# Performance work log

Measured on AMD Instinct MI355X. Metric: run time of the kernel, lower is better.

The kernel has to match this reference:

```python
import jax, jax.numpy as jnp
import numpy as np

B, T, D, H, Dh, ROT = 2, 2048, 2048, 16, 128, 64
DFF = 4 * D
EPS = 1e-5
NEG = -1e9


def setup_inputs() -> dict:
    key = jax.random.key(0)
    ks = jax.random.split(key, 8)
    s = lambda k, shape, sc: jax.random.normal(k, shape, jnp.float32) * sc
    return {
        "x": s(ks[0], (B, T, D), 1.0),
        "ln_scale": jnp.ones((D,), jnp.float32),
        "ln_offset": jnp.zeros((D,), jnp.float32),
        "wq": s(ks[1], (D, D), 0.02),
        "wk": s(ks[2], (D, D), 0.02),
        "wv": s(ks[3], (D, D), 0.02),
        "wo": s(ks[4], (D, D), 0.02),
        "w1": s(ks[5], (D, DFF), 0.02),
        "b1": jnp.zeros((DFF,), jnp.float32),
        "w2": s(ks[6], (DFF, D), 0.02),
        "b2": jnp.zeros((D,), jnp.float32),
    }


def reference(x, ln_scale, ln_offset, wq, wk, wv, wo, w1, b1, w2, b2):
    def ln(h):  # ReplicatedLayerNorm, fp32 internal; note: same params used twice (shared self.norm)
        h32 = h.astype(jnp.float32)
        m = jnp.mean(h32, axis=-1, keepdims=True)
        v = jnp.var(h32, axis=-1, keepdims=True)
        y = (h32 - m) * jax.lax.rsqrt(v + EPS)
        return (y * ln_scale + ln_offset).astype(h.dtype)

    xn = ln(x)
    q = (xn @ wq).reshape(B, T, H, Dh)
    k = (xn @ wk).reshape(B, T, H, Dh)
    v = (xn @ wv).reshape(B, T, H, Dh)

    # GPT-J interleaved RoPE on first ROT dims
    pos = jnp.arange(T, dtype=jnp.float32)
    inv_freq = 1.0 / (10000.0 ** (jnp.arange(0, ROT, 2, dtype=jnp.float32) / ROT))
    freqs = pos[:, None] * inv_freq[None, :]            # (T, ROT/2)
    cos = jnp.repeat(jnp.cos(freqs), 2, axis=-1)[None, :, None, :]  # (1,T,1,ROT)
    sin = jnp.repeat(jnp.sin(freqs), 2, axis=-1)[None, :, None, :]

    def rope(t):
        tr, tp = t[..., :ROT], t[..., ROT:]
        x1 = tr[..., 0::2]
        x2 = tr[..., 1::2]
        rot_half = jnp.stack((-x2, x1), axis=-1).reshape(tr.shape)
        return jnp.concatenate([tr * cos + rot_half * sin, tp], axis=-1)

    q, k = rope(q), rope(k)

    scale = 1.0 / jnp.sqrt(jnp.float32(Dh))
    scores = jnp.einsum('bthd,bshd->bhts', q, k) * scale
    mask = jnp.where(jnp.tril(jnp.ones((T, T), bool)), 0.0, NEG).astype(scores.dtype)
    w = jax.nn.softmax(scores + mask, axis=-1)
    ctx = jnp.einsum('bhts,bshd->bthd', w, v).reshape(B, T, D)
    x1_ = x + ctx @ wo

    xn2 = ln(x1_)
    h = jax.nn.gelu(xn2.astype(jnp.float32) @ w1 + b1)  # default approximate gelu, as in source
    ff = (h @ w2 + b2).astype(x.dtype)
    return x1_ + ff
```

## Files before the change

kernel.cpp:

```cpp
#include <hip/hip_runtime.h>
#include <hip/hip_bf16.h>

#define B_   2
#define T_   2048
#define D_   2048
#define H_   16
#define DH_  128
#define DFF_ 8192

typedef __attribute__((ext_vector_type(8))) short bf16x8;
typedef __attribute__((ext_vector_type(4))) float f32x4;

__device__ __forceinline__ short f2bf(float f) {
    __hip_bfloat16 h = __float2bfloat16(f);
    return *reinterpret_cast<short*>(&h);
}

__device__ __forceinline__ void gload_lds16(const void* g, void* l) {
    __builtin_amdgcn_global_load_lds(
        (const __attribute__((address_space(1))) void*)g,
        (__attribute__((address_space(3))) void*)l,
        16, 0, 0);
}

__device__ __forceinline__ float gelu_tanh(float x) {
    float x3 = x * x * x;
    return 0.5f * x * (1.f + tanhf(0.7978845608028654f * (x + 0.044715f * x3)));
}

#define MFMA32(a, b, c) __builtin_amdgcn_mfma_f32_16x16x32_bf16((a), (b), (c), 0, 0, 0)

__global__ __launch_bounds__(256) void transpose_cvt(const float* __restrict__ in,
                                                     __hip_bfloat16* __restrict__ out,
                                                     int K, int N, int out_ld, int out_row0)
{
    __shared__ float t[32][65];
    const int n0 = blockIdx.x * 64, k0 = blockIdx.y * 32;
    const int tid = threadIdx.x;
    {
        int kr = tid >> 4;
        int nc = (tid & 15) * 4;
        const float* src = in + (size_t)(k0 + kr) * N + n0 + nc;
        float4 a = *reinterpret_cast<const float4*>(src);
        float4 b = *reinterpret_cast<const float4*>(src + (size_t)16 * N);
        t[kr][nc] = a.x; t[kr][nc + 1] = a.y; t[kr][nc + 2] = a.z; t[kr][nc + 3] = a.w;
        t[kr + 16][nc] = b.x; t[kr + 16][nc + 1] = b.y; t[kr + 16][nc + 2] = b.z; t[kr + 16][nc + 3] = b.w;
    }
    __syncthreads();
    {
        int n  = tid >> 2;
        int kc = (tid & 3) * 8;
        __hip_bfloat16 ob[8];
#pragma unroll
        for (int j = 0; j < 8; ++j) ob[j] = __float2bfloat16(t[kc + j][n]);
        *reinterpret_cast<uint4*>(out + (size_t)(out_row0 + n0 + n) * out_ld + k0 + kc) =
            *reinterpret_cast<uint4*>(ob);
    }
}

__global__ __launch_bounds__(256) void ln_kernel(const float* __restrict__ x,
                                                 const float* __restrict__ sc,
                                                 const float* __restrict__ of,
                                                 __hip_bfloat16* __restrict__ out)
{
    int row = blockIdx.x, tid = threadIdx.x;
    const float* xr = x + (size_t)row * D_;
    float4 v0 = reinterpret_cast<const float4*>(xr)[tid * 2];
    float4 v1 = reinterpret_cast<const float4*>(xr)[tid * 2 + 1];
    float vv[8] = {v0.x, v0.y, v0.z, v0.w, v1.x, v1.y, v1.z, v1.w};
    float s = 0.f, ss = 0.f;
#pragma unroll
    for (int j = 0; j < 8; ++j) { s += vv[j]; ss += vv[j] * vv[j]; }
    for (int o = 32; o; o >>= 1) { s += __shfl_down(s, o); ss += __shfl_down(ss, o); }
    __shared__ float red[8];
    int wid = tid >> 6, lane = tid & 63;
    if (!lane) { red[wid] = s; red[4 + wid] = ss; }
    __syncthreads();
    s  = red[0] + red[1] + red[2] + red[3];
    ss = red[4] + red[5] + red[6] + red[7];
    float mean = s * (1.f / D_);
    float var  = ss * (1.f / D_) - mean * mean;
    float rstd = rsqrtf(var + 1e-5f);
    int c0 = tid * 8;
    __hip_bfloat16 ob[8];
#pragma unroll
    for (int j = 0; j < 8; ++j)
        ob[j] = __float2bfloat16((vv[j] - mean) * rstd * sc[c0 + j] + of[c0 + j]);
    *reinterpret_cast<uint4*>(out + (size_t)row * D_ + c0) = *reinterpret_cast<uint4*>(ob);
}

template<int EPI, int BM>
__global__ __launch_bounds__(512, 2) void gemm8p(
    const __hip_bfloat16* __restrict__ A, const __hip_bfloat16* __restrict__ BT,
    void* __restrict__ Cout, const float* __restrict__ bias,
    const float* __restrict__ resid, int M, int N, int K)
{
    constexpr int MFR = BM / 32;
    constexpr int AUL = BM / 128;
    constexpr int VMC = AUL + 2;
    __shared__ short As[2 * 2 * BM * 32];
    __shared__ short Bs[2 * 2 * 256 * 32];

    const int tid = threadIdx.x;
    const int wid = tid >> 6, lane = tid & 63;
    const int lo = lane & 15, hi = lane >> 4;
    const int wr = wid >> 2, wc = wid & 3;

    const int gx = gridDim.x;
    const int nwg = gx * gridDim.y;
    const int bid = blockIdx.y * gx + blockIdx.x;
    const int swz = (bid & 7) * (nwg >> 3) + (bid >> 3);
    const int m0 = (swz / gx) * BM, n0 = (swz % gx) * 256;

    auto stageA = [&](int tt, int ks) {
#pragma unroll
        for (int l = 0; l < AUL; ++l) {
            int c    = l * 512 + tid;
            int row  = c >> 2, ksub = c & 3;
            int kc   = tt * 64 + ks * 32 + ((ksub ^ ((row >> 1) & 3)) << 3);
            int c0   = l * 512 + wid * 64;
            gload_lds16(A + (size_t)(m0 + row) * K + kc,
                        (char*)As + ((tt & 1) * 2 + ks) * (BM * 64) + c0 * 16);
        }
    };
    auto stageB = [&](int tt, int ks) {
#pragma unroll
        for (int l = 0; l < 2; ++l) {
            int c    = l * 512 + tid;
            int row  = c >> 2, ksub = c & 3;
            int kc   = tt * 64 + ks * 32 + ((ksub ^ ((row >> 1) & 3)) << 3);
            int c0   = l * 512 + wid * 64;
            gload_lds16(BT + (size_t)(n0 + row) * K + kc,
                        (char*)Bs + ((tt & 1) * 2 + ks) * 16384 + c0 * 16);
        }
    };

    const int fsw  = (hi ^ ((lo >> 1) & 3)) << 4;
    const int arow = wr * (BM / 2) + lo;
    const int brow = wc * 64 + lo;

    f32x4 acc[MFR][4] = {};
    const int NT = K >> 6;

    stageA(0, 0); stageB(0, 0); stageA(0, 1); stageB(0, 1);
    asm volatile("s_waitcnt vmcnt(%0)" :: "i"(VMC) : "memory");
    __builtin_amdgcn_s_barrier();
    __builtin_amdgcn_sched_barrier(0);

#define PHASE_MFMA(J)                                                         \
        __builtin_amdgcn_s_barrier();                                         \
        asm volatile("s_waitcnt lgkmcnt(0)" ::: "memory");                    \
        __builtin_amdgcn_sched_barrier(0);                                    \
        __builtin_amdgcn_s_setprio(1);                                        \
        _Pragma("unroll")                                                     \
        for (int m = 0; m < MFR; ++m) {                                       \
            acc[m][J]     = MFMA32(af[m], b0, acc[m][J]);                     \
            acc[m][J + 1] = MFMA32(af[m], b1, acc[m][J + 1]);                 \
        }                                                                     \
        __builtin_amdgcn_s_setprio(0);

#pragma unroll 2
    for (int t = 0; t < NT; ++t) {
        const int bsel = t & 1;
        const bool pf = (t + 1 < NT);
        const char* Ab = (const char*)As + bsel * (2 * BM * 64);
        const char* Bb = (const char*)Bs + bsel * 32768;
        bf16x8 af[MFR], b0, b1;

#pragma unroll
        for (int m = 0; m < MFR; ++m)
            af[m] = *reinterpret_cast<const bf16x8*>(Ab + (arow + m * 16) * 64 + fsw);
        b0 = *reinterpret_cast<const bf16x8*>(Bb + brow * 64 + fsw);
        b1 = *reinterpret_cast<const bf16x8*>(Bb + (brow + 16) * 64 + fsw);
        if (pf) stageA(t + 1, 0);
        PHASE_MFMA(0)
        __builtin_amdgcn_s_barrier();
        __builtin_amdgcn_sched_barrier(0);

        b0 = *reinterpret_cast<const bf16x8*>(Bb + (brow + 32) * 64 + fsw);
        b1 = *reinterpret_cast<const bf16x8*>(Bb + (brow + 48) * 64 + fsw);
        if (pf) stageB(t + 1, 0);
        PHASE_MFMA(2)
        asm volatile("s_waitcnt vmcnt(%0)" :: "i"(VMC) : "memory");
        __builtin_amdgcn_s_barrier();
        __builtin_amdgcn_sched_barrier(0);

#pragma unroll
        for (int m = 0; m < MFR; ++m)
            af[m] = *reinterpret_cast<const bf16x8*>(Ab + BM * 64 + (arow + m * 16) * 64 + fsw);
        b0 = *reinterpret_cast<const bf16x8*>(Bb + 16384 + brow * 64 + fsw);
        b1 = *reinterpret_cast<const bf16x8*>(Bb + 16384 + (brow + 16) * 64 + fsw);
        if (pf) stageA(t + 1, 1);
        PHASE_MFMA(0)
        __builtin_amdgcn_s_barrier();
        __builtin_amdgcn_sched_barrier(0);

        b0 = *reinterpret_cast<const bf16x8*>(Bb + 16384 + (brow + 32) * 64 + fsw);
        b1 = *reinterpret_cast<const bf16x8*>(Bb + 16384 + (brow + 48) * 64 + fsw);
        if (pf) stageB(t + 1, 1);
        PHASE_MFMA(2)
        asm volatile("s_waitcnt vmcnt(%0)" :: "i"(VMC) : "memory");
        __builtin_amdgcn_s_barrier();
        __builtin_amdgcn_sched_barrier(0);
    }
#undef PHASE_MFMA

    float* Cf = (float*)Cout;
    __hip_bfloat16* Cb = (__hip_bfloat16*)Cout;
#pragma unroll
    for (int m = 0; m < MFR; ++m) {
        int rbase = m0 + wr * (BM / 2) + m * 16 + hi * 4;
#pragma unroll
        for (int j = 0; j < 4; ++j) {
            int col = n0 + wc * 64 + (j >> 1) * 32 + (j & 1) * 16 + lo;
            float bv = (EPI == 2 || EPI == 3) ? bias[col] : 0.f;
#pragma unroll
            for (int i = 0; i < 4; ++i) {
                size_t idx = (size_t)(rbase + i) * N + col;
                float v = acc[m][j][i];
                if (EPI == 2 || EPI == 3) v += bv;
                if (EPI == 2) v = gelu_tanh(v);
                if (EPI == 1 || EPI == 3) v += resid[idx];
                if (EPI == 0 || EPI == 2) Cb[idx] = __float2bfloat16(v);
                else                      Cf[idx] = v;
            }
        }
    }
}

__global__ __launch_bounds__(256) void rope_kernel(__hip_bfloat16* __restrict__ qkv)
{
    int idx = blockIdx.x * 256 + threadIdx.x;
    int p  = idx & 31;
    int h  = (idx >> 5) & (H_ - 1);
    int bt = idx >> 9;
    int t  = bt & (T_ - 1);
    float invf = exp2f((float)p * -0.4152410118609203f);
    float fr = (float)t * invf;
    float cs, sn;
    __sincosf(fr, &sn, &cs);
    size_t base = (size_t)bt * (3 * D_) + h * DH_ + 2 * p;
#pragma unroll
    for (int qk = 0; qk < 2; ++qk) {
        uint* pp = reinterpret_cast<uint*>(qkv + base + qk * D_);
        uint u = *pp;
        float x1 = __uint_as_float(u << 16);
        float x2 = __uint_as_float(u & 0xffff0000u);
        short r0 = f2bf(x1 * cs - x2 * sn);
        short r1 = f2bf(x2 * cs + x1 * sn);
        *pp = ((uint)(unsigned short)r0) | (((uint)(unsigned short)r1) << 16);
    }
}

__global__ __launch_bounds__(512) void attn_kernel(const __hip_bfloat16* __restrict__ qkv,
                                                   __hip_bfloat16* __restrict__ ctx)
{
    constexpr int LDQ = 3 * D_;
    constexpr int SV  = 68;
    constexpr int SP  = 68;

    int idx = blockIdx.y * 16 + blockIdx.x;
    int swz = (idx & 7) * 64 + (idx >> 3);
    const int bh  = swz >> 4;
    const int bxr = 15 - (swz & 15);
    const int b = bh >> 4, h = bh & 15;
    const int tq0 = bxr * 128;

    const int tid = threadIdx.x, wid = tid >> 6, lane = tid & 63;
    const int lo = lane & 15, hi = lane >> 4;
    const int t0 = tq0 + wid * 16;

    __shared__ short Ks[2][64 * 128];
    __shared__ short VsT[128 * SV];
    __shared__ short Ps[8][16 * SP];

    const __hip_bfloat16* qrow = qkv + (size_t)(b * T_ + t0 + lo) * LDQ + h * DH_;
    bf16x8 qf[4];
#pragma unroll
    for (int dk = 0; dk < 4; ++dk)
        qf[dk] = *reinterpret_cast<const bf16x8*>(qrow + dk * 32 + hi * 8);

    f32x4 octx[8] = {};
    float mreg[4] = {-1e30f, -1e30f, -1e30f, -1e30f};
    float lreg[4] = {0.f, 0.f, 0.f, 0.f};

    const size_t kvrow0 = (size_t)(b * T_) * LDQ + h * DH_;
    const int nst = 2 * (bxr + 1);

    bf16x8 vr[2];

#define STAGE_K(s0v, buf)                                                     \
    do {                                                                      \
        _Pragma("unroll")                                                     \
        for (int i = 0; i < 2; ++i) {                                         \
            int c    = i * 512 + tid;                                         \
            int sr   = c >> 4;                                                \
            int cbs  = ((c & 15) * 16) ^ ((sr & 7) << 4);                     \
            gload_lds16(qkv + kvrow0 + (size_t)((s0v) + sr) * LDQ + D_ + (cbs >> 1), \
                        &Ks[buf][c * 8]);                                     \
        }                                                                     \
    } while (0)

#define LOAD_V(s0v)                                                           \
    do {                                                                      \
        _Pragma("unroll")                                                     \
        for (int it = 0; it < 2; ++it) {                                      \
            int c = it * 512 + tid;                                           \
            int s = c >> 4, dc = c & 15;                                      \
            vr[it] = *reinterpret_cast<const bf16x8*>(                        \
                qkv + kvrow0 + (size_t)((s0v) + s) * LDQ + 2 * D_ + dc * 8);  \
        }                                                                     \
    } while (0)

    STAGE_K(0, 0);
    LOAD_V(0);

    for (int st = 0; st < nst; ++st) {
        const int s0 = st * 64;
        const int cur = st & 1;
        __syncthreads();

#pragma unroll
        for (int it = 0; it < 2; ++it) {
            int c = it * 512 + tid;
            int s = c >> 4, dc = c & 15;
            int sswz = s ^ ((dc & 15) << 2);
            short* dst = &VsT[(dc * 8) * SV + sswz];
#pragma unroll
            for (int j = 0; j < 8; ++j)
                dst[j * SV] = vr[it][j];
        }
        if (st + 1 < nst) {
            STAGE_K(s0 + 64, cur ^ 1);
            LOAD_V(s0 + 64);
        }
        asm volatile("s_waitcnt lgkmcnt(0)" ::: "memory");
        __builtin_amdgcn_s_barrier();
        __builtin_amdgcn_sched_barrier(0);

        f32x4 sfr[4] = {};
        __builtin_amdgcn_s_setprio(1);
#pragma unroll
        for (int f = 0; f < 4; ++f) {
            int srow = f * 16 + lo;
            int sw = (srow & 7) << 4;
#pragma unroll
            for (int dk = 0; dk < 4; ++dk) {
                bf16x8 kf = *reinterpret_cast<const bf16x8*>(
                    (const char*)&Ks[cur][0] + srow * 256 + ((dk * 64 + hi * 16) ^ sw));
                sfr[f] = MFMA32(qf[dk], kf, sfr[f]);
            }
        }
        __builtin_amdgcn_s_setprio(0);

        const float qsc = 0.08838834764831845f;
#pragma unroll
        for (int f = 0; f < 4; ++f)
#pragma unroll
            for (int i = 0; i < 4; ++i)
                sfr[f][i] *= qsc;
        if (st >= nst - 2) {
#pragma unroll
            for (int f = 0; f < 4; ++f)
#pragma unroll
                for (int i = 0; i < 4; ++i)
                    if (s0 + f * 16 + lo > t0 + hi * 4 + i) sfr[f][i] = -1e30f;
        }

        float ps[4];
#pragma unroll
        for (int i = 0; i < 4; ++i) {
            float v = fmaxf(fmaxf(sfr[0][i], sfr[1][i]), fmaxf(sfr[2][i], sfr[3][i]));
            v = fmaxf(v, __shfl_xor(v, 1));
            v = fmaxf(v, __shfl_xor(v, 2));
            v = fmaxf(v, __shfl_xor(v, 4));
            v = fmaxf(v, __shfl_xor(v, 8));
            float mn = fmaxf(mreg[i], v);
            ps[i] = __expf(mreg[i] - mn);
            mreg[i] = mn;
        }
#pragma unroll
        for (int f = 0; f < 4; ++f)
#pragma unroll
            for (int i = 0; i < 4; ++i)
                sfr[f][i] = __expf(sfr[f][i] - mreg[i]);
#pragma unroll
        for (int i = 0; i < 4; ++i) {
            float v = sfr[0][i] + sfr[1][i] + sfr[2][i] + sfr[3][i];
            v += __shfl_xor(v, 1); v += __shfl_xor(v, 2);
            v += __shfl_xor(v, 4); v += __shfl_xor(v, 8);
            lreg[i] = lreg[i] * ps[i] + v;
        }
#pragma unroll
        for (int f8 = 0; f8 < 8; ++f8)
#pragma unroll
            for (int i = 0; i < 4; ++i)
                octx[f8][i] *= ps[i];

        short* pw = &Ps[wid][0];
#pragma unroll
        for (int f = 0; f < 4; ++f)
#pragma unroll
            for (int i = 0; i < 4; ++i)
                pw[(hi * 4 + i) * SP + f * 16 + lo] = f2bf(sfr[f][i]);
        asm volatile("s_waitcnt lgkmcnt(0)" ::: "memory");
        __builtin_amdgcn_sched_barrier(0);

#pragma unroll
        for (int ks = 0; ks < 2; ++ks) {
            union { bf16x8 v; uint2 u[2]; } pa;
            pa.u[0] = *reinterpret_cast<const uint2*>(pw + lo * SP + ks * 32 + hi * 4);
            pa.u[1] = *reinterpret_cast<const uint2*>(pw + lo * SP + ks * 32 + 16 + hi * 4);
            __builtin_amdgcn_s_setprio(1);
#pragma unroll
            for (int f8 = 0; f8 < 8; ++f8) {
                int d = f8 * 16 + lo;
                int sw2 = ((d >> 3) & 15) << 2;
                const short* vrow = &VsT[d * SV];
                union { bf16x8 v; uint2 u[2]; } vb;
                vb.u[0] = *reinterpret_cast<const uint2*>(vrow + ((ks * 32 + hi * 4) ^ sw2));
                vb.u[1] = *reinterpret_cast<const uint2*>(vrow + ((ks * 32 + 16 + hi * 4) ^ sw2));
                octx[f8] = MFMA32(pa.v, vb.v, octx[f8]);
            }
            __builtin_amdgcn_s_setprio(0);
        }
    }
#undef STAGE_K
#undef LOAD_V

#pragma unroll
    for (int i = 0; i < 4; ++i) {
        float inv = 1.f / lreg[i];
        size_t rb = (size_t)(b * T_ + t0 + hi * 4 + i) * D_ + h * DH_;
#pragma unroll
        for (int f8 = 0; f8 < 8; ++f8)
            ctx[rb + f8 * 16 + lo] = __float2bfloat16(octx[f8][i] * inv);
    }
}

extern "C" void kernel_launch(void* const* d_in, const int* in_sizes, int n_in,
                              void* d_out, int out_size, void* d_ws, size_t ws_size,
                              hipStream_t stream)
{
    (void)in_sizes; (void)n_in; (void)out_size; (void)ws_size;
    const float* x   = (const float*)d_in[0];
    const float* lns = (const float*)d_in[1];
    const float* lno = (const float*)d_in[2];
    const float* wq  = (const float*)d_in[3];
    const float* wk  = (const float*)d_in[4];
    const float* wv  = (const float*)d_in[5];
    const float* wo  = (const float*)d_in[6];
    const float* w1  = (const float*)d_in[7];
    const float* b1  = (const float*)d_in[8];
    const float* w2  = (const float*)d_in[9];
    const float* b2  = (const float*)d_in[10];
    float* out = (float*)d_out;

    char* ws = (char*)d_ws;
    __hip_bfloat16* wqkvT = (__hip_bfloat16*)(ws);
    __hip_bfloat16* woT   = (__hip_bfloat16*)(ws + 25165824);
    __hip_bfloat16* w1T   = (__hip_bfloat16*)(ws + 33554432);
    __hip_bfloat16* w2T   = (__hip_bfloat16*)(ws + 67108864);
    __hip_bfloat16* xn    = (__hip_bfloat16*)(ws + 100663296);
    __hip_bfloat16* qkv   = (__hip_bfloat16*)(ws + 117440512);
    __hip_bfloat16* hbuf  = qkv;
    __hip_bfloat16* ctx   = (__hip_bfloat16*)(ws + 167772160);
    float*          x1    = (float*)(ws + 184549376);

    transpose_cvt<<<dim3(32, 64),  256, 0, stream>>>(wq, wqkvT, 2048, 2048, 2048, 0);
    transpose_cvt<<<dim3(32, 64),  256, 0, stream>>>(wk, wqkvT, 2048, 2048, 2048, 2048);
    transpose_cvt<<<dim3(32, 64),  256, 0, stream>>>(wv, wqkvT, 2048, 2048, 2048, 4096);
    transpose_cvt<<<dim3(32, 64),  256, 0, stream>>>(wo, woT,   2048, 2048, 2048, 0);
    transpose_cvt<<<dim3(128, 64), 256, 0, stream>>>(w1, w1T,   2048, 8192, 2048, 0);
    transpose_cvt<<<dim3(32, 256), 256, 0, stream>>>(w2, w2T,   8192, 2048, 8192, 0);

    ln_kernel<<<4096, 256, 0, stream>>>(x, lns, lno, xn);
    gemm8p<0, 128><<<dim3(24, 32), 512, 0, stream>>>(xn, wqkvT, qkv, nullptr, nullptr, 4096, 6144, 2048);
    rope_kernel<<<8192, 256, 0, stream>>>(qkv);
    attn_kernel<<<dim3(16, 32), 512, 0, stream>>>(qkv, ctx);
    gemm8p<1, 128><<<dim3(8, 32), 512, 0, stream>>>(ctx, woT, x1, nullptr, x, 4096, 2048, 2048);
    ln_kernel<<<4096, 256, 0, stream>>>(x1, lns, lno, xn);
    gemm8p<2, 256><<<dim3(32, 16), 512, 0, stream>>>(xn, w1T, hbuf, b1, nullptr, 4096, 8192, 2048);
    gemm8p<3, 128><<<dim3(8, 32), 512, 0, stream>>>(hbuf, w2T, out, b2, x1, 4096, 2048, 8192);
}
```

Baseline: 802.6 us.

## Compute transposed S in attention to keep P in registers, dropping LDS round-trip

Swaps the MFMA operand order so the score tile is produced transposed (keys along rows, queries along lanes). The probabilities can then be packed straight into the A-operand of the PV MFMA without staging through per-wave shared memory. Row max and sum now need only two cross-lane shuffles, plus broadcasts of the rescale factor and normalizer. This removes the Ps LDS buffer, its writes, reads and wait. The cost is extra shuffles, and the result depends on the MFMA register layout matching the expected operand layout.

```diff
diff --git a/kernel.cpp b/kernel.cpp
--- a/kernel.cpp
+++ b/kernel.cpp
@@ -257,7 +257,6 @@
 {
     constexpr int LDQ = 3 * D_;
     constexpr int SV  = 68;
-    constexpr int SP  = 68;
 
     int idx = blockIdx.y * 16 + blockIdx.x;
     int swz = (idx & 7) * 64 + (idx >> 3);
@@ -272,7 +271,6 @@
 
     __shared__ short Ks[2][64 * 128];
     __shared__ short VsT[128 * SV];
-    __shared__ short Ps[8][16 * SP];
 
     const __hip_bfloat16* qrow = qkv + (size_t)(b * T_ + t0 + lo) * LDQ + h * DH_;
     bf16x8 qf[4];
@@ -281,8 +279,7 @@
         qf[dk] = *reinterpret_cast<const bf16x8*>(qrow + dk * 32 + hi * 8);
 
     f32x4 octx[8] = {};
-    float mreg[4] = {-1e30f, -1e30f, -1e30f, -1e30f};
-    float lreg[4] = {0.f, 0.f, 0.f, 0.f};
+    float mreg = -1e30f, lreg = 0.f;
 
     const size_t kvrow0 = (size_t)(b * T_) * LDQ + h * DH_;
     const int nst = 2 * (bxr + 1);
@@ -348,7 +345,7 @@
             for (int dk = 0; dk < 4; ++dk) {
                 bf16x8 kf = *reinterpret_cast<const bf16x8*>(
                     (const char*)&Ks[cur][0] + srow * 256 + ((dk * 64 + hi * 16) ^ sw));
-                sfr[f] = MFMA32(qf[dk], kf, sfr[f]);
+                sfr[f] = MFMA32(kf, qf[dk], sfr[f]);
             }
         }
         __builtin_amdgcn_s_setprio(0);
@@ -364,53 +361,50 @@
             for (int f = 0; f < 4; ++f)
 #pragma unroll
                 for (int i = 0; i < 4; ++i)
-                    if (s0 + f * 16 + lo > t0 + hi * 4 + i) sfr[f][i] = -1e30f;
-        }
-
-        float ps[4];
-#pragma unroll
-        for (int i = 0; i < 4; ++i) {
-            float v = fmaxf(fmaxf(sfr[0][i], sfr[1][i]), fmaxf(sfr[2][i], sfr[3][i]));
-            v = fmaxf(v, __shfl_xor(v, 1));
-            v = fmaxf(v, __shfl_xor(v, 2));
-            v = fmaxf(v, __shfl_xor(v, 4));
-            v = fmaxf(v, __shfl_xor(v, 8));
-            float mn = fmaxf(mreg[i], v);
-            ps[i] = __expf(mreg[i] - mn);
-            mreg[i] = mn;
-        }
+                    if (s0 + f * 16 + hi * 4 + i > t0 + lo) sfr[f][i] = -1e30f;
+        }
+
+        float mx = -1e30f;
 #pragma unroll
         for (int f = 0; f < 4; ++f)
 #pragma unroll
             for (int i = 0; i < 4; ++i)
-                sfr[f][i] = __expf(sfr[f][i] - mreg[i]);
-#pragma unroll
-        for (int i = 0; i < 4; ++i) {
-            float v = sfr[0][i] + sfr[1][i] + sfr[2][i] + sfr[3][i];
-            v += __shfl_xor(v, 1); v += __shfl_xor(v, 2);
-            v += __shfl_xor(v, 4); v += __shfl_xor(v, 8);
-            lreg[i] = lreg[i] * ps[i] + v;
-        }
+                mx = fmaxf(mx, sfr[f][i]);
+        mx = fmaxf(mx, __shfl_xor(mx, 16));
+        mx = fmaxf(mx, __shfl_xor(mx, 32));
+        float mn = fmaxf(mreg, mx);
+        float ps = __expf(mreg - mn);
+        mreg = mn;
+        float sum = 0.f;
+#pragma unroll
+        for (int f = 0; f < 4; ++f)
+#pragma unroll
+            for (int i = 0; i < 4; ++i) {
+                sfr[f][i] = __expf(sfr[f][i] - mn);
+                sum += sfr[f][i];
+            }
+        sum += __shfl_xor(sum, 16);
+        sum += __shfl_xor(sum, 32);
+        lreg = lreg * ps + sum;
+
+        float psq[4];
+#pragma unroll
+        for (int i = 0; i < 4; ++i)
+            psq[i] = __shfl(ps, hi * 4 + i);
 #pragma unroll
         for (int f8 = 0; f8 < 8; ++f8)
 #pragma unroll
             for (int i = 0; i < 4; ++i)
-                octx[f8][i] *= ps[i];
-
-        short* pw = &Ps[wid][0];
-#pragma unroll
-        for (int f = 0; f < 4; ++f)
-#pragma unroll
-            for (int i = 0; i < 4; ++i)
-                pw[(hi * 4 + i) * SP + f * 16 + lo] = f2bf(sfr[f][i]);
-        asm volatile("s_waitcnt lgkmcnt(0)" ::: "memory");
-        __builtin_amdgcn_sched_barrier(0);
+                octx[f8][i] *= psq[i];
 
 #pragma unroll
         for (int ks = 0; ks < 2; ++ks) {
-            union { bf16x8 v; uint2 u[2]; } pa;
-            pa.u[0] = *reinterpret_cast<const uint2*>(pw + lo * SP + ks * 32 + hi * 4);
-            pa.u[1] = *reinterpret_cast<const uint2*>(pw + lo * SP + ks * 32 + 16 + hi * 4);
+            union { bf16x8 v; short s[8]; } pa;
+#pragma unroll
+            for (int j = 0; j < 4; ++j) {
+                pa.s[j]     = f2bf(sfr[2 * ks][j]);
+                pa.s[j + 4] = f2bf(sfr[2 * ks + 1][j]);
+            }
             __builtin_amdgcn_s_setprio(1);
 #pragma unroll
             for (int f8 = 0; f8 < 8; ++f8) {
@@ -428,13 +422,16 @@
 #undef STAGE_K
 #undef LOAD_V
 
+    float linv[4];
+#pragma unroll
+    for (int i = 0; i < 4; ++i)
+        linv[i] = 1.f / __shfl(lreg, hi * 4 + i);
 #pragma unroll
     for (int i = 0; i < 4; ++i) {
-        float inv = 1.f / lreg[i];
         size_t rb = (size_t)(b * T_ + t0 + hi * 4 + i) * D_ + h * DH_;
 #pragma unroll
         for (int f8 = 0; f8 < 8; ++f8)
-            ctx[rb + f8 * 16 + lo] = __float2bfloat16(octx[f8][i] * inv);
+            ctx[rb + f8 * 16 + lo] = __float2bfloat16(octx[f8][i] * linv[i]);
     }
 }
 
```

Measured after the change: 769.6 us. 1.04x faster.
